# Optimization experiments

Measured on AMD Instinct MI355X. Metric: run time of the kernel, lower is better.

## Reference

```python
import jax, jax.numpy as jnp
import numpy as np

B, N, C, H = 2, 2048, 256, 8
HD = C // H  # 32


def _pairwise_sq_dist(x, y):
    # x,y: [B,N,3] -> [B,N,N] squared euclidean distance
    x2 = jnp.sum(x * x, axis=-1)  # [B,N]
    y2 = jnp.sum(y * y, axis=-1)  # [B,N]
    xy = jnp.einsum('bnd,bmd->bnm', x, y)
    return x2[:, :, None] + y2[:, None, :] - 2.0 * xy


def setup_inputs() -> dict:
    key = jax.random.key(0)
    ks = jax.random.split(key, 12)
    s = 0.02
    return {
        'feature': jax.random.normal(ks[0], (B, N, C), jnp.float32),
        'points': jax.random.normal(ks[1], (B, N, 3), jnp.float32),
        'Wq': jax.random.normal(ks[2], (C, H * HD), jnp.float32) * s,
        'bq': jnp.zeros((H * HD,), jnp.float32),
        'Wk': jax.random.normal(ks[3], (C, H * HD), jnp.float32) * s,
        'bk': jnp.zeros((H * HD,), jnp.float32),
        'Wv': jax.random.normal(ks[4], (C, H * HD), jnp.float32) * s,
        'bv': jnp.zeros((H * HD,), jnp.float32),
        'Wo': jax.random.normal(ks[5], (H * HD, C), jnp.float32) * s,
        'bo': jnp.zeros((C,), jnp.float32),
        'ln_g': jnp.ones((C,), jnp.float32),
        'ln_b': jnp.zeros((C,), jnp.float32),
    }


def reference(feature, points, Wq, bq, Wk, bk, Wv, bv, Wo, bo, ln_g, ln_b):
    xyz = points[..., 0:3]
    dist = _pairwise_sq_dist(xyz, xyz)  # [B,N,N] geometric bias

    q = (feature @ Wq + bq).reshape(B, N, H, HD)
    k = (feature @ Wk + bk).reshape(B, N, H, HD)
    v = (feature @ Wv + bv).reshape(B, N, H, HD)

    # distance-biased multi-head attention (Geoglobal_FPT)
    logits = jnp.einsum('bnhd,bmhd->bhnm', q, k) / jnp.sqrt(jnp.float32(HD))
    logits = logits - dist[:, None, :, :]  # closer points attend more
    attn = jax.nn.softmax(logits, axis=-1)
    out = jnp.einsum('bhnm,bmhd->bnhd', attn, v).reshape(B, N, H * HD)
    out = out @ Wo + bo

    # residual + post-LayerNorm
    f = feature + out
    mu = jnp.mean(f, axis=-1, keepdims=True)
    var = jnp.mean(jnp.square(f - mu), axis=-1, keepdims=True)
    f = (f - mu) * jax.lax.rsqrt(var + 1e-5) * ln_g + ln_b
    return f
```

## Files before the change

### kernel.cpp

```cpp
#include <hip/hip_runtime.h>
#include <hip/hip_bf16.h>

#define B_ 2
#define N_ 2048
#define C_ 256
#define H_ 8
#define HD_ 32

typedef __bf16 bhalf;
typedef bhalf bhalf8 __attribute__((ext_vector_type(8)));
typedef bhalf bhalf4 __attribute__((ext_vector_type(4)));
typedef float floatx4 __attribute__((ext_vector_type(4)));
typedef short short4v __attribute__((ext_vector_type(4)));

__device__ __forceinline__ floatx4 mfma16x16x16bf16(bhalf4 a, bhalf4 b, floatx4 c) {
#if __has_builtin(__builtin_amdgcn_mfma_f32_16x16x16_bf16)
    return __builtin_amdgcn_mfma_f32_16x16x16_bf16(a, b, c, 0, 0, 0);
#else
    return __builtin_amdgcn_mfma_f32_16x16x16bf16_1k(
        __builtin_bit_cast(short4v, a), __builtin_bit_cast(short4v, b), c, 0, 0, 0);
#endif
}

__global__ __launch_bounds__(256) void prep_all(
    const float* __restrict__ Wq, const float* __restrict__ Wk,
    const float* __restrict__ Wv, const float* __restrict__ Wo,
    const float* __restrict__ pts, const float* __restrict__ feat,
    bhalf* __restrict__ Wtb, bhalf* __restrict__ qext,
    bhalf* __restrict__ kext, bhalf* __restrict__ fb)
{
    __shared__ float T[64][65];
    const int bx = blockIdx.x;
    const int t = threadIdx.x;
    if (bx < 64) {
        const int wsel = bx >> 4;
        const float* W = wsel == 0 ? Wq : (wsel == 1 ? Wk : (wsel == 2 ? Wv : Wo));
        bhalf* dst = Wtb + (size_t)wsel * (C_ * C_);
        const int tile = bx & 15;
        const int kt = (tile >> 2) * 64, nt = (tile & 3) * 64;
        const int c4 = (t & 15) * 4;
#pragma unroll
        for (int i = 0; i < 4; ++i) {
            const int r = (t >> 4) + i * 16;
            const float4 w = *(const float4*)&W[(kt + r) * C_ + nt + c4];
            T[r][c4 + 0] = w.x; T[r][c4 + 1] = w.y; T[r][c4 + 2] = w.z; T[r][c4 + 3] = w.w;
        }
        __syncthreads();
#pragma unroll
        for (int i = 0; i < 4; ++i) {
            const int n = (t >> 4) + i * 16;
            bhalf4 o;
            o[0] = (bhalf)T[c4 + 0][n]; o[1] = (bhalf)T[c4 + 1][n];
            o[2] = (bhalf)T[c4 + 2][n]; o[3] = (bhalf)T[c4 + 3][n];
            *(bhalf4*)&dst[(nt + n) * C_ + kt + c4] = o;
        }
    } else if (bx < 80) {
        const int i = (bx - 64) * 256 + t;
        const float x = pts[i * 3 + 0], y = pts[i * 3 + 1], z = pts[i * 3 + 2];
        const float nn = x * x + y * y + z * z;
        const bhalf hi = (bhalf)nn;
        const bhalf lo = (bhalf)(nn - (float)hi);
        bhalf8 qe, ke;
        qe[0] = (bhalf)(2.f * x); qe[1] = (bhalf)(2.f * y); qe[2] = (bhalf)(2.f * z);
        qe[3] = (bhalf)(-(float)hi); qe[4] = (bhalf)(-(float)lo);
        qe[5] = (bhalf)1.f; qe[6] = (bhalf)1.f; qe[7] = (bhalf)0.f;
        ke[0] = (bhalf)x; ke[1] = (bhalf)y; ke[2] = (bhalf)z;
        ke[3] = (bhalf)1.f; ke[4] = (bhalf)1.f;
        ke[5] = (bhalf)(-(float)hi); ke[6] = (bhalf)(-(float)lo); ke[7] = (bhalf)0.f;
        *(bhalf8*)&qext[(size_t)i * 8] = qe;
        *(bhalf8*)&kext[(size_t)i * 8] = ke;
    } else {
        const int idx = ((bx - 80) * 256 + t) * 4;
        const float4 f = *(const float4*)&feat[idx];
        bhalf4 o;
        o[0] = (bhalf)f.x; o[1] = (bhalf)f.y; o[2] = (bhalf)f.z; o[3] = (bhalf)f.w;
        *(bhalf4*)&fb[idx] = o;
    }
}

__global__ __launch_bounds__(256) void qkv_gemm(
    const bhalf* __restrict__ fb, const bhalf* __restrict__ Wtb,
    const float* __restrict__ bq, const float* __restrict__ bk,
    const float* __restrict__ bv,
    bhalf* __restrict__ qs, bhalf* __restrict__ kg, bhalf* __restrict__ vt)
{
    __shared__ __align__(16) bhalf Alds[2][32][72];
    __shared__ __align__(16) bhalf Blds[2][64][72];

    const int tid = threadIdx.x;
    const int wave = tid >> 6, lane = tid & 63;
    const int quad = lane >> 4, l16 = lane & 15;
    const int m0 = blockIdx.x * 32;
    const int which = blockIdx.y >> 2;
    const int n0 = (blockIdx.y & 3) * 64;
    const bhalf* Wt = Wtb + (size_t)which * (C_ * C_);
    const int mw = (wave & 1) * 16;
    const int cw = (wave >> 1) * 32;

    const floatx4 zacc = {0.f, 0.f, 0.f, 0.f};
    floatx4 acc[2] = {zacc, zacc};

    const int arow = tid >> 3, aoff = (tid & 7) * 8;
    const int brow = tid >> 2, boff = (tid & 3) * 16;

    bhalf8 ra  = *(const bhalf8*)&fb[(m0 + arow) * C_ + aoff];
    bhalf8 rb0 = *(const bhalf8*)&Wt[(n0 + brow) * C_ + boff];
    bhalf8 rb1 = *(const bhalf8*)&Wt[(n0 + brow) * C_ + boff + 8];
    *(bhalf8*)&Alds[0][arow][aoff] = ra;
    *(bhalf8*)&Blds[0][brow][boff] = rb0;
    *(bhalf8*)&Blds[0][brow][boff + 8] = rb1;

    int cur = 0;
    for (int kci = 0; kci < 4; ++kci) {
        __syncthreads();
        if (kci < 3) {
            const int kc = (kci + 1) * 64;
            ra  = *(const bhalf8*)&fb[(m0 + arow) * C_ + kc + aoff];
            rb0 = *(const bhalf8*)&Wt[(n0 + brow) * C_ + kc + boff];
            rb1 = *(const bhalf8*)&Wt[(n0 + brow) * C_ + kc + boff + 8];
        }
        const bhalf8 a0 = *(const bhalf8*)&Alds[cur][mw + l16][quad * 8];
        const bhalf8 a1 = *(const bhalf8*)&Alds[cur][mw + l16][32 + quad * 8];
#pragma unroll
        for (int f = 0; f < 2; ++f) {
            const bhalf8 b0 = *(const bhalf8*)&Blds[cur][cw + f * 16 + l16][quad * 8];
            const bhalf8 b1 = *(const bhalf8*)&Blds[cur][cw + f * 16 + l16][32 + quad * 8];
            acc[f] = __builtin_amdgcn_mfma_f32_16x16x32_bf16(a0, b0, acc[f], 0, 0, 0);
            acc[f] = __builtin_amdgcn_mfma_f32_16x16x32_bf16(a1, b1, acc[f], 0, 0, 0);
        }
        if (kci < 3) {
            *(bhalf8*)&Alds[cur ^ 1][arow][aoff] = ra;
            *(bhalf8*)&Blds[cur ^ 1][brow][boff] = rb0;
            *(bhalf8*)&Blds[cur ^ 1][brow][boff + 8] = rb1;
        }
        cur ^= 1;
    }

    const float scale = 0.17677669529663687f;
    const float* bias = which == 0 ? bq : (which == 1 ? bk : bv);
#pragma unroll
    for (int f = 0; f < 2; ++f) {
        const int cg = n0 + cw + f * 16 + l16;
        const float bi = bias[cg];
        const int hh = cg >> 5, dd = cg & 31;
        const int m = m0 + mw + quad * 4;
        const int bb = m >> 11, nn = m & (N_ - 1);
        if (which == 2) {
            bhalf4 vw;
#pragma unroll
            for (int r = 0; r < 4; ++r) vw[r] = (bhalf)(acc[f][r] + bi);
            *(bhalf4*)&vt[(((size_t)(bb * H_ + hh) * (N_ / 64) + (nn >> 6)) * HD_ + dd) * 64 + (nn & 63)] = vw;
        } else {
#pragma unroll
            for (int r = 0; r < 4; ++r) {
                const float val = acc[f][r] + bi;
                if (which == 0)
                    qs[((size_t)(bb * H_ + hh) * N_ + nn + r) * HD_ + dd] = (bhalf)(val * scale);
                else
                    kg[((size_t)(bb * H_ + hh) * N_ + nn + r) * HD_ + dd] = (bhalf)val;
            }
        }
    }
}

__global__ __launch_bounds__(256) void attn_kernel(
    const bhalf* __restrict__ qs, const bhalf* __restrict__ kg,
    const bhalf* __restrict__ vt, const bhalf* __restrict__ qext,
    const bhalf* __restrict__ kext,
    bhalf* __restrict__ po, float* __restrict__ pl, int spbits)
{
    __shared__ __align__(16) bhalf Ks[2][64][40];
    __shared__ __align__(16) bhalf Vts[2][32][72];
    __shared__ __align__(16) bhalf Kes[2][64][8];

    const int tid = threadIdx.x;
    const int wave = tid >> 6, lane = tid & 63;
    const int quad = lane >> 4, l16 = lane & 15;
    const int n0 = blockIdx.x * 128;
    const int h = blockIdx.y;
    const int sp = blockIdx.z & ((1 << spbits) - 1);
    const int b = blockIdx.z >> spbits;
    const int bh = b * H_ + h;

    const int qrow0 = n0 + wave * 32 + l16;
    const int qrow1 = qrow0 + 16;
    const bhalf8 bq0 = *(const bhalf8*)&qs[((size_t)bh * N_ + qrow0) * HD_ + quad * 8];
    const bhalf8 bq1 = *(const bhalf8*)&qs[((size_t)bh * N_ + qrow1) * HD_ + quad * 8];
    bhalf8 zv8;
#pragma unroll
    for (int j = 0; j < 8; ++j) zv8[j] = (bhalf)0.f;
    const bhalf8 bqe0 = (quad == 0)
        ? *(const bhalf8*)&qext[(size_t)(b * N_ + qrow0) * 8] : zv8;
    const bhalf8 bqe1 = (quad == 0)
        ? *(const bhalf8*)&qext[(size_t)(b * N_ + qrow1) * 8] : zv8;

    const floatx4 zacc = {0.f, 0.f, 0.f, 0.f};
    floatx4 o00 = zacc, o01 = zacc, o10 = zacc, o11 = zacc;
    float ls0 = 0.f, ls1 = 0.f;

    const int skey = tid >> 2, sseg = tid & 3;
    const int vd = tid >> 3, vks = tid & 7;
    const int ekey = tid >> 1, eoff = (tid & 1) * 4;
    const int iters = (N_ >> spbits) / 64;
    const int mbase = sp * (N_ >> spbits);

    bhalf8 rk = *(const bhalf8*)&kg[((size_t)bh * N_ + mbase + skey) * HD_ + sseg * 8];
    bhalf8 rv = *(const bhalf8*)&vt[(((size_t)bh * (N_ / 64) + (mbase >> 6)) * HD_ + vd) * 64 + vks * 8];
    bhalf4 re;
    if (tid < 128) re = *(const bhalf4*)&kext[(size_t)(b * N_ + mbase + ekey) * 8 + eoff];
    *(bhalf8*)&Ks[0][skey][sseg * 8] = rk;
    *(bhalf8*)&Vts[0][vd][vks * 8] = rv;
    if (tid < 128) *(bhalf4*)&Kes[0][ekey][eoff] = re;

    int cur = 0;
    for (int it = 0; it < iters; ++it) {
        __syncthreads();
        if (it + 1 < iters) {
            const int m1 = mbase + (it + 1) * 64;
            rk = *(const bhalf8*)&kg[((size_t)bh * N_ + m1 + skey) * HD_ + sseg * 8];
            rv = *(const bhalf8*)&vt[(((size_t)bh * (N_ / 64) + (m1 >> 6)) * HD_ + vd) * 64 + vks * 8];
            if (tid < 128) re = *(const bhalf4*)&kext[(size_t)(b * N_ + m1 + ekey) * 8 + eoff];
        }
#pragma unroll
        for (int mt = 0; mt < 4; ++mt) {
            const bhalf8 ak_ = *(const bhalf8*)&Ks[cur][mt * 16 + l16][quad * 8];
            const bhalf8 ake = (quad == 0)
                ? *(const bhalf8*)&Kes[cur][mt * 16 + l16][0] : zv8;
            floatx4 st0 = __builtin_amdgcn_mfma_f32_16x16x32_bf16(ak_, bq0, zacc, 0, 0, 0);
            st0 = __builtin_amdgcn_mfma_f32_16x16x32_bf16(ake, bqe0, st0, 0, 0, 0);
            floatx4 st1 = __builtin_amdgcn_mfma_f32_16x16x32_bf16(ak_, bq1, zacc, 0, 0, 0);
            st1 = __builtin_amdgcn_mfma_f32_16x16x32_bf16(ake, bqe1, st1, 0, 0, 0);
            bhalf4 pt0, pt1;
#pragma unroll
            for (int r = 0; r < 4; ++r) {
                const float p0 = __expf(st0[r]);
                const float p1 = __expf(st1[r]);
                ls0 += p0; ls1 += p1;
                pt0[r] = (bhalf)p0; pt1[r] = (bhalf)p1;
            }
            const bhalf4 av0 = *(const bhalf4*)&Vts[cur][l16][mt * 16 + quad * 4];
            const bhalf4 av1 = *(const bhalf4*)&Vts[cur][16 + l16][mt * 16 + quad * 4];
            o00 = mfma16x16x16bf16(av0, pt0, o00);
            o01 = mfma16x16x16bf16(av1, pt0, o01);
            o10 = mfma16x16x16bf16(av0, pt1, o10);
            o11 = mfma16x16x16bf16(av1, pt1, o11);
        }
        if (it + 1 < iters) {
            *(bhalf8*)&Ks[cur ^ 1][skey][sseg * 8] = rk;
            *(bhalf8*)&Vts[cur ^ 1][vd][vks * 8] = rv;
            if (tid < 128) *(bhalf4*)&Kes[cur ^ 1][ekey][eoff] = re;
        }
        cur ^= 1;
    }

    ls0 += __shfl_xor(ls0, 16); ls0 += __shfl_xor(ls0, 32);
    ls1 += __shfl_xor(ls1, 16); ls1 += __shfl_xor(ls1, 32);

    const size_t pobase = (size_t)sp * ((size_t)B_ * H_ * N_ * HD_) + (size_t)bh * N_ * HD_;
    bhalf4 w00, w01, w10, w11;
#pragma unroll
    for (int r = 0; r < 4; ++r) {
        w00[r] = (bhalf)o00[r]; w01[r] = (bhalf)o01[r];
        w10[r] = (bhalf)o10[r]; w11[r] = (bhalf)o11[r];
    }
    *(bhalf4*)&po[pobase + (size_t)qrow0 * HD_ + quad * 4] = w00;
    *(bhalf4*)&po[pobase + (size_t)qrow0 * HD_ + 16 + quad * 4] = w01;
    *(bhalf4*)&po[pobase + (size_t)qrow1 * HD_ + quad * 4] = w10;
    *(bhalf4*)&po[pobase + (size_t)qrow1 * HD_ + 16 + quad * 4] = w11;
    if (lane < 16)
        pl[(size_t)sp * (B_ * H_ * N_) + (size_t)bh * N_ + qrow0] = ls0;
    else if (lane < 32)
        pl[(size_t)sp * (B_ * H_ * N_) + (size_t)bh * N_ + qrow1] = ls1;
}

__global__ __launch_bounds__(512) void outln_gemm(
    const bhalf* __restrict__ po, const float* __restrict__ pl,
    const bhalf* __restrict__ Wot, const float* __restrict__ bo,
    const float* __restrict__ feat, const float* __restrict__ g,
    const float* __restrict__ bb, float* __restrict__ out, int splits)
{
    __shared__ __align__(16) bhalf Alds[16][264];
    __shared__ __align__(16) bhalf Blds[2][256][40];
    __shared__ float rden[16][8];
    __shared__ float wsum[8][16][2];
    __shared__ float stats[16][2];

    const int tid = threadIdx.x;
    const int wave = tid >> 6, lane = tid & 63;
    const int quad = lane >> 4, l16 = lane & 15;
    const int row0 = blockIdx.x * 16;

    if (tid < 128) {
        const int m = tid >> 3, hh = tid & 7;
        const int grow = row0 + m;
        const int b = grow >> 11, n = grow & (N_ - 1);
        float den = 0.f;
        for (int sp = 0; sp < splits; ++sp)
            den += pl[(size_t)sp * (B_ * H_ * N_) + (size_t)(b * H_ + hh) * N_ + n];
        rden[m][hh] = 1.f / den;
    }
    __syncthreads();

    {
        const int m = tid >> 5, seg = tid & 31;
        const int hh = seg >> 2, d0 = (seg & 3) * 8;
        const int grow = row0 + m;
        const int b = grow >> 11, n = grow & (N_ - 1);
        const size_t idx = ((size_t)(b * H_ + hh) * N_ + n) * HD_ + d0;
        float num[8];
#pragma unroll
        for (int j = 0; j < 8; ++j) num[j] = 0.f;
        for (int sp = 0; sp < splits; ++sp) {
            const bhalf8 p0 = *(const bhalf8*)&po[(size_t)sp * ((size_t)B_ * H_ * N_ * HD_) + idx];
#pragma unroll
            for (int j = 0; j < 8; ++j) num[j] += (float)p0[j];
        }
        const float r = rden[m][hh];
        bhalf8 a0;
#pragma unroll
        for (int j = 0; j < 8; ++j) a0[j] = (bhalf)(num[j] * r);
        *(bhalf8*)&Alds[m][seg * 8] = a0;
    }

    const floatx4 zacc = {0.f, 0.f, 0.f, 0.f};
    floatx4 acc[2] = {zacc, zacc};

    const int brow = tid >> 1, bkoff = (tid & 1) * 16;
    bhalf8 rb0 = *(const bhalf8*)&Wot[brow * C_ + bkoff];
    bhalf8 rb1 = *(const bhalf8*)&Wot[brow * C_ + bkoff + 8];
    *(bhalf8*)&Blds[0][brow][bkoff]     = rb0;
    *(bhalf8*)&Blds[0][brow][bkoff + 8] = rb1;

    int cur = 0;
    for (int kci = 0; kci < 8; ++kci) {
        __syncthreads();
        if (kci < 7) {
            const bhalf* wp = &Wot[brow * C_ + (kci + 1) * 32 + bkoff];
            rb0 = *(const bhalf8*)(wp);
            rb1 = *(const bhalf8*)(wp + 8);
        }
        const bhalf8 af = *(const bhalf8*)&Alds[l16][kci * 32 + quad * 8];
#pragma unroll
        for (int f = 0; f < 2; ++f) {
            const bhalf8 bfr = *(const bhalf8*)&Blds[cur][wave * 32 + f * 16 + l16][quad * 8];
            acc[f] = __builtin_amdgcn_mfma_f32_16x16x32_bf16(af, bfr, acc[f], 0, 0, 0);
        }
        if (kci < 7) {
            *(bhalf8*)&Blds[cur ^ 1][brow][bkoff]     = rb0;
            *(bhalf8*)&Blds[cur ^ 1][brow][bkoff + 8] = rb1;
        }
        cur ^= 1;
    }

    float fv[2][4];
    float s1[4] = {0.f, 0.f, 0.f, 0.f}, s2[4] = {0.f, 0.f, 0.f, 0.f};
#pragma unroll
    for (int f = 0; f < 2; ++f) {
        const int col = wave * 32 + f * 16 + l16;
        const float bic = bo[col];
#pragma unroll
        for (int r = 0; r < 4; ++r) {
            const int m = quad * 4 + r;
            const float x = acc[f][r] + bic + feat[(row0 + m) * C_ + col];
            fv[f][r] = x;
            s1[r] += x; s2[r] += x * x;
        }
    }
#pragma unroll
    for (int r = 0; r < 4; ++r) {
        for (int o = 1; o < 16; o <<= 1) {
            s1[r] += __shfl_xor(s1[r], o);
            s2[r] += __shfl_xor(s2[r], o);
        }
    }
    if (l16 == 0) {
#pragma unroll
        for (int r = 0; r < 4; ++r) {
            wsum[wave][quad * 4 + r][0] = s1[r];
            wsum[wave][quad * 4 + r][1] = s2[r];
        }
    }
    __syncthreads();
    if (tid < 16) {
        float a = 0.f, bsq = 0.f;
#pragma unroll
        for (int w = 0; w < 8; ++w) { a += wsum[w][tid][0]; bsq += wsum[w][tid][1]; }
        const float mu = a * (1.f / C_);
        const float var = bsq * (1.f / C_) - mu * mu;
        stats[tid][0] = mu;
        stats[tid][1] = rsqrtf(var + 1e-5f);
    }
    __syncthreads();
#pragma unroll
    for (int f = 0; f < 2; ++f) {
        const int col = wave * 32 + f * 16 + l16;
        const float gc = g[col], bc = bb[col];
#pragma unroll
        for (int r = 0; r < 4; ++r) {
            const int m = quad * 4 + r;
            out[(row0 + m) * C_ + col] = (fv[f][r] - stats[m][0]) * stats[m][1] * gc + bc;
        }
    }
}

extern "C" void kernel_launch(void* const* d_in, const int* in_sizes, int n_in,
                              void* d_out, int out_size, void* d_ws, size_t ws_size,
                              hipStream_t stream) {
    const float* feat = (const float*)d_in[0];
    const float* pts  = (const float*)d_in[1];
    const float* Wq   = (const float*)d_in[2];
    const float* bq   = (const float*)d_in[3];
    const float* Wk   = (const float*)d_in[4];
    const float* bk   = (const float*)d_in[5];
    const float* Wv   = (const float*)d_in[6];
    const float* bv   = (const float*)d_in[7];
    const float* Wo   = (const float*)d_in[8];
    const float* bo   = (const float*)d_in[9];
    const float* lng  = (const float*)d_in[10];
    const float* lnb  = (const float*)d_in[11];

    char* w = (char*)d_ws;
    bhalf* Wtb  = (bhalf*)(w);
    bhalf* fb   = (bhalf*)(w + 524288);
    bhalf* qs   = (bhalf*)(w + 2621440);
    bhalf* kg   = (bhalf*)(w + 4718592);
    bhalf* vtp  = (bhalf*)(w + 6815744);
    bhalf* qext = (bhalf*)(w + 8912896);
    bhalf* kext = (bhalf*)(w + 8978432);
    float* pl   = (float*)(w + 9043968);
    bhalf* po   = (bhalf*)(w + 9568256);

    const int spbits = (ws_size >= 17956864u) ? 2 : 1;
    const int splits = 1 << spbits;

    prep_all<<<80 + B_ * N_ * C_ / 1024, 256, 0, stream>>>(
        Wq, Wk, Wv, Wo, pts, feat, Wtb, qext, kext, fb);
    qkv_gemm<<<dim3(B_ * N_ / 32, 12), 256, 0, stream>>>(
        fb, Wtb, bq, bk, bv, qs, kg, vtp);
    attn_kernel<<<dim3(N_ / 128, H_, B_ << spbits), 256, 0, stream>>>(
        qs, kg, vtp, qext, kext, po, pl, spbits);
    outln_gemm<<<B_ * N_ / 16, 512, 0, stream>>>(
        po, pl, Wtb + 3 * (C_ * C_), bo, feat, lng, lnb, (float*)d_out, splits);
}
```

Baseline: 119.0 us.

## Load K/V tiles directly from global memory and shrink distance-bias MFMA

The attention kernel no longer stages K, V^T and the key-extension tile through double-buffered shared memory with block-wide barriers. Each wave now loads its MFMA fragments straight from global memory, relying on L1/L2 to serve the four waves that read the same tiles. The distance-bias term also moves from a padded 16x16x32 MFMA to a 16x16x16 one. This removes LDS traffic and __syncthreads, at the cost of redundant global loads across waves and no explicit software prefetch of the next tile.

Result: slower. 141.3 us (+18.7%).

```diff
diff --git a/kernel.cpp b/kernel.cpp
--- a/kernel.cpp
+++ b/kernel.cpp
@@ -169,10 +169,6 @@
     const bhalf* __restrict__ kext,
     bhalf* __restrict__ po, float* __restrict__ pl, int spbits)
 {
-    __shared__ __align__(16) bhalf Ks[2][64][40];
-    __shared__ __align__(16) bhalf Vts[2][32][72];
-    __shared__ __align__(16) bhalf Kes[2][64][8];
-
     const int tid = threadIdx.x;
     const int wave = tid >> 6, lane = tid & 63;
     const int quad = lane >> 4, l16 = lane & 15;
@@ -186,50 +182,43 @@
     const int qrow1 = qrow0 + 16;
     const bhalf8 bq0 = *(const bhalf8*)&qs[((size_t)bh * N_ + qrow0) * HD_ + quad * 8];
     const bhalf8 bq1 = *(const bhalf8*)&qs[((size_t)bh * N_ + qrow1) * HD_ + quad * 8];
-    bhalf8 zv8;
-#pragma unroll
-    for (int j = 0; j < 8; ++j) zv8[j] = (bhalf)0.f;
-    const bhalf8 bqe0 = (quad == 0)
-        ? *(const bhalf8*)&qext[(size_t)(b * N_ + qrow0) * 8] : zv8;
-    const bhalf8 bqe1 = (quad == 0)
-        ? *(const bhalf8*)&qext[(size_t)(b * N_ + qrow1) * 8] : zv8;
+    bhalf4 zv4;
+#pragma unroll
+    for (int j = 0; j < 4; ++j) zv4[j] = (bhalf)0.f;
+    const bhalf4 bqe0 = (quad < 2)
+        ? *(const bhalf4*)&qext[(size_t)(b * N_ + qrow0) * 8 + quad * 4] : zv4;
+    const bhalf4 bqe1 = (quad < 2)
+        ? *(const bhalf4*)&qext[(size_t)(b * N_ + qrow1) * 8 + quad * 4] : zv4;
 
     const floatx4 zacc = {0.f, 0.f, 0.f, 0.f};
     floatx4 o00 = zacc, o01 = zacc, o10 = zacc, o11 = zacc;
     float ls0 = 0.f, ls1 = 0.f;
 
-    const int skey = tid >> 2, sseg = tid & 3;
-    const int vd = tid >> 3, vks = tid & 7;
-    const int ekey = tid >> 1, eoff = (tid & 1) * 4;
     const int iters = (N_ >> spbits) / 64;
     const int mbase = sp * (N_ >> spbits);
 
-    bhalf8 rk = *(const bhalf8*)&kg[((size_t)bh * N_ + mbase + skey) * HD_ + sseg * 8];
-    bhalf8 rv = *(const bhalf8*)&vt[(((size_t)bh * (N_ / 64) + (mbase >> 6)) * HD_ + vd) * 64 + vks * 8];
-    bhalf4 re;
-    if (tid < 128) re = *(const bhalf4*)&kext[(size_t)(b * N_ + mbase + ekey) * 8 + eoff];
-    *(bhalf8*)&Ks[0][skey][sseg * 8] = rk;
-    *(bhalf8*)&Vts[0][vd][vks * 8] = rv;
-    if (tid < 128) *(bhalf4*)&Kes[0][ekey][eoff] = re;
-
-    int cur = 0;
     for (int it = 0; it < iters; ++it) {
-        __syncthreads();
-        if (it + 1 < iters) {
-            const int m1 = mbase + (it + 1) * 64;
-            rk = *(const bhalf8*)&kg[((size_t)bh * N_ + m1 + skey) * HD_ + sseg * 8];
-            rv = *(const bhalf8*)&vt[(((size_t)bh * (N_ / 64) + (m1 >> 6)) * HD_ + vd) * 64 + vks * 8];
-            if (tid < 128) re = *(const bhalf4*)&kext[(size_t)(b * N_ + m1 + ekey) * 8 + eoff];
-        }
+        const int m0 = mbase + it * 64;
+        const bhalf* kb = &kg[((size_t)bh * N_ + m0) * HD_];
+        const bhalf* vb = &vt[((size_t)bh * (N_ / 64) + (m0 >> 6)) * (HD_ * 64)];
+        const bhalf* eb = &kext[(size_t)(b * N_ + m0) * 8];
+
+        bhalf8 kf[4];
+        bhalf4 ef[4], vf0[4], vf1[4];
 #pragma unroll
         for (int mt = 0; mt < 4; ++mt) {
-            const bhalf8 ak_ = *(const bhalf8*)&Ks[cur][mt * 16 + l16][quad * 8];
-            const bhalf8 ake = (quad == 0)
-                ? *(const bhalf8*)&Kes[cur][mt * 16 + l16][0] : zv8;
-            floatx4 st0 = __builtin_amdgcn_mfma_f32_16x16x32_bf16(ak_, bq0, zacc, 0, 0, 0);
-            st0 = __builtin_amdgcn_mfma_f32_16x16x32_bf16(ake, bqe0, st0, 0, 0, 0);
-            floatx4 st1 = __builtin_amdgcn_mfma_f32_16x16x32_bf16(ak_, bq1, zacc, 0, 0, 0);
-            st1 = __builtin_amdgcn_mfma_f32_16x16x32_bf16(ake, bqe1, st1, 0, 0, 0);
+            kf[mt] = *(const bhalf8*)&kb[(mt * 16 + l16) * HD_ + quad * 8];
+            ef[mt] = (quad < 2)
+                ? *(const bhalf4*)&eb[(mt * 16 + l16) * 8 + quad * 4] : zv4;
+            vf0[mt] = *(const bhalf4*)&vb[l16 * 64 + mt * 16 + quad * 4];
+            vf1[mt] = *(const bhalf4*)&vb[(16 + l16) * 64 + mt * 16 + quad * 4];
+        }
+#pragma unroll
+        for (int mt = 0; mt < 4; ++mt) {
+            floatx4 st0 = __builtin_amdgcn_mfma_f32_16x16x32_bf16(kf[mt], bq0, zacc, 0, 0, 0);
+            st0 = mfma16x16x16bf16(ef[mt], bqe0, st0);
+            floatx4 st1 = __builtin_amdgcn_mfma_f32_16x16x32_bf16(kf[mt], bq1, zacc, 0, 0, 0);
+            st1 = mfma16x16x16bf16(ef[mt], bqe1, st1);
             bhalf4 pt0, pt1;
 #pragma unroll
             for (int r = 0; r < 4; ++r) {
@@ -238,19 +227,11 @@
                 ls0 += p0; ls1 += p1;
                 pt0[r] = (bhalf)p0; pt1[r] = (bhalf)p1;
             }
-            const bhalf4 av0 = *(const bhalf4*)&Vts[cur][l16][mt * 16 + quad * 4];
-            const bhalf4 av1 = *(const bhalf4*)&Vts[cur][16 + l16][mt * 16 + quad * 4];
-            o00 = mfma16x16x16bf16(av0, pt0, o00);
-            o01 = mfma16x16x16bf16(av1, pt0, o01);
-            o10 = mfma16x16x16bf16(av0, pt1, o10);
-            o11 = mfma16x16x16bf16(av1, pt1, o11);
-        }
-        if (it + 1 < iters) {
-            *(bhalf8*)&Ks[cur ^ 1][skey][sseg * 8] = rk;
-            *(bhalf8*)&Vts[cur ^ 1][vd][vks * 8] = rv;
-            if (tid < 128) *(bhalf4*)&Kes[cur ^ 1][ekey][eoff] = re;
-        }
-        cur ^= 1;
+            o00 = mfma16x16x16bf16(vf0[mt], pt0, o00);
+            o01 = mfma16x16x16bf16(vf1[mt], pt0, o01);
+            o10 = mfma16x16x16bf16(vf0[mt], pt1, o10);
+            o11 = mfma16x16x16bf16(vf1[mt], pt1, o11);
+        }
     }
 
     ls0 += __shfl_xor(ls0, 16); ls0 += __shfl_xor(ls0, 32);
```
